# Performance work log

Hardware: AMD Instinct MI355X
Metric: run time of the kernel (lower is better)

## Reference

```python
import jax, jax.numpy as jnp
import numpy as np

N_ATOM_FEATS = 64
N_RBF = 10
N_CONV = 3
N_HIDDEN = 64
N_NODES = 50000
N_EDGES = 800000
N_GRAPHS = 512


def setup_inputs() -> dict:
    key = jax.random.key(0)
    ks = jax.random.split(key, 32)
    d = {}
    d["x_ids"] = jax.random.randint(ks[0], (N_NODES,), 0, 95)
    d["edge_index"] = jax.random.randint(ks[1], (2, N_EDGES), 0, N_NODES)
    d["edge_attr"] = jax.random.uniform(ks[2], (N_EDGES,), jnp.float32) * 6.0  # distances in [0,6)
    d["batch"] = jnp.sort(jax.random.randint(ks[3], (N_NODES,), 0, N_GRAPHS))
    # parameters
    def lin(k, fan_in, shape):
        return jax.random.normal(k, shape, jnp.float32) / np.sqrt(fan_in)
    d["emb"] = jax.random.normal(ks[4], (95, N_ATOM_FEATS), jnp.float32)
    d["blk_W1"] = lin(ks[5], N_ATOM_FEATS, (N_CONV, N_ATOM_FEATS, N_ATOM_FEATS))
    d["blk_b1"] = jnp.zeros((N_CONV, N_ATOM_FEATS), jnp.float32)
    d["blk_We"] = lin(ks[6], N_RBF, (N_CONV, N_RBF, N_ATOM_FEATS))
    d["blk_be"] = jnp.zeros((N_CONV, N_ATOM_FEATS), jnp.float32)
    d["blk_W2"] = lin(ks[7], N_ATOM_FEATS, (N_CONV, N_ATOM_FEATS, N_ATOM_FEATS))
    d["blk_b2"] = jnp.zeros((N_CONV, N_ATOM_FEATS), jnp.float32)
    d["Ws"] = lin(ks[8], N_ATOM_FEATS, (N_ATOM_FEATS, 2 * N_HIDDEN))
    d["bs"] = jnp.zeros((2 * N_HIDDEN,), jnp.float32)
    d["Wbg1"] = lin(ks[9], 2 * N_HIDDEN, (2 * N_HIDDEN, N_HIDDEN))
    d["bbg1"] = jnp.zeros((N_HIDDEN,), jnp.float32)
    d["Wbg2"] = lin(ks[10], N_HIDDEN, (N_HIDDEN, 1))
    d["bbg2"] = jnp.zeros((1,), jnp.float32)
    d["Weh1"] = lin(ks[11], 2 * N_HIDDEN, (2 * N_HIDDEN, N_HIDDEN))
    d["beh1"] = jnp.zeros((N_HIDDEN,), jnp.float32)
    d["Weh2"] = lin(ks[12], N_HIDDEN, (N_HIDDEN, 1))
    d["beh2"] = jnp.zeros((1,), jnp.float32)
    return d


def reference(x_ids, edge_index, edge_attr, batch, emb,
              blk_W1, blk_b1, blk_We, blk_be, blk_W2, blk_b2,
              Ws, bs, Wbg1, bbg1, Wbg2, bbg2, Weh1, beh1, Weh2, beh2):
    src, dst = edge_index[0], edge_index[1]
    # embedding lookup [N, F]
    x = emb[x_ids]
    # Gaussian smearing RBF: [E, n_rbf]
    offset = jnp.linspace(0.0, 6.0, N_RBF).astype(edge_attr.dtype)
    coeff = -0.5 / (offset[1] - offset[0]) ** 2
    e = jnp.exp(coeff * (edge_attr[:, None] - offset) ** 2)
    # interaction blocks (SchNet-style CFConv with residual)
    for i in range(N_CONV):
        h = x @ blk_W1[i] + blk_b1[i]                     # [N, F]
        f = e @ blk_We[i] + blk_be[i]                     # [E, F] edge filters
        m = h[src] * f                                    # [E, F] messages
        agg = jax.ops.segment_sum(m, dst, num_segments=N_NODES)
        x = x + agg @ blk_W2[i] + blk_b2[i]
        x = jax.nn.softplus(x)
    # global mean pool over graphs
    sums = jax.ops.segment_sum(x, batch, num_segments=N_GRAPHS)
    cnts = jax.ops.segment_sum(jnp.ones((x.shape[0],), x.dtype), batch, num_segments=N_GRAPHS)
    c = sums / jnp.maximum(cnts, 1.0)[:, None]
    c = jax.nn.relu(c @ Ws + bs)                          # [G, 2H]
    out_bg = jax.nn.relu(c @ Wbg1 + bbg1) @ Wbg2 + bbg2   # [G, 1]
    out_eh = jax.nn.relu(c @ Weh1 + beh1) @ Weh2 + beh2   # [G, 1]
    return (out_bg, out_eh)
```

## Files before the change

### kernel.cpp

```cpp
#include <hip/hip_runtime.h>
#include <hip/hip_fp16.h>
#include <cstddef>


#define RBF_C0 1.0f
#define RBF_C1 0.60653065971f
#define RBF_C2 0.13533528324f
#define RBF_C3 0.011108996538f
#define RBF_C4 3.3546262790e-4f
#define RBF_C5 3.7266531720e-6f
#define RBF_C6 1.5229979745e-8f
#define RBF_C7 2.2897348457e-11f
#define RBF_C8 1.2664165549e-14f
#define RBF_C9 2.5767043600e-18f

__device__ __forceinline__ float softplusf(float v) {
    return fmaxf(v, 0.0f) + log1pf(__expf(-fabsf(v)));
}

__device__ __forceinline__ float row_gemv(const float4* __restrict__ xr,
                                          const float w[64], float bj) {
    float a0 = bj, a1 = 0.f, a2 = 0.f, a3 = 0.f;
#pragma unroll
    for (int q = 0; q < 4; ++q) {
        float4 v0 = xr[4 * q + 0], v1 = xr[4 * q + 1];
        float4 v2 = xr[4 * q + 2], v3 = xr[4 * q + 3];
        a0 = fmaf(v0.x, w[16 * q + 0], a0);  a0 = fmaf(v0.y, w[16 * q + 1], a0);
        a0 = fmaf(v0.z, w[16 * q + 2], a0);  a0 = fmaf(v0.w, w[16 * q + 3], a0);
        a1 = fmaf(v1.x, w[16 * q + 4], a1);  a1 = fmaf(v1.y, w[16 * q + 5], a1);
        a1 = fmaf(v1.z, w[16 * q + 6], a1);  a1 = fmaf(v1.w, w[16 * q + 7], a1);
        a2 = fmaf(v2.x, w[16 * q + 8], a2);  a2 = fmaf(v2.y, w[16 * q + 9], a2);
        a2 = fmaf(v2.z, w[16 * q + 10], a2); a2 = fmaf(v2.w, w[16 * q + 11], a2);
        a3 = fmaf(v3.x, w[16 * q + 12], a3); a3 = fmaf(v3.y, w[16 * q + 13], a3);
        a3 = fmaf(v3.z, w[16 * q + 14], a3); a3 = fmaf(v3.w, w[16 * q + 15], a3);
    }
    return (a0 + a1) + (a2 + a3);
}

__device__ __forceinline__ float filt_ab(const float wp[10], float bj, float A, float B) {
    float P = wp[9];
    P = fmaf(B, P, wp[8]); P = fmaf(B, P, wp[7]); P = fmaf(B, P, wp[6]);
    P = fmaf(B, P, wp[5]); P = fmaf(B, P, wp[4]); P = fmaf(B, P, wp[3]);
    P = fmaf(B, P, wp[2]); P = fmaf(B, P, wp[1]); P = fmaf(B, P, wp[0]);
    return fmaf(A, P, bj);
}

__global__ void k_pre(const int* __restrict__ dst, int* __restrict__ deg,
                      const int* __restrict__ batch, int* __restrict__ gstart,
                      const int* __restrict__ ids, const float* __restrict__ emb,
                      const float* __restrict__ W1, const float* __restrict__ b1,
                      float* __restrict__ x, __half* __restrict__ hA,
                      int n_edges, int n_nodes, int n_graphs) {
    int tid = blockIdx.x * blockDim.x + threadIdx.x;
    int nth = gridDim.x * blockDim.x;
    for (int e = tid; e < n_edges; e += nth) atomicAdd(&deg[dst[e]], 1);
    for (int n = tid; n < n_nodes; n += nth) {
        int b = batch[n];
        int prev = (n == 0) ? -1 : batch[n - 1];
        for (int g = prev + 1; g <= b; ++g) gstart[g] = n;
        if (n == n_nodes - 1)
            for (int g = b + 1; g <= n_graphs; ++g) gstart[g] = n_nodes;
    }
    int lane = threadIdx.x & 63;
    int gw = __builtin_amdgcn_readfirstlane(tid >> 6);
    int nw = nth >> 6;
    float w[64];
#pragma unroll
    for (int k = 0; k < 64; ++k) w[k] = W1[k * 64 + lane];
    float bj = b1[lane];
    for (int n = gw; n < n_nodes; n += nw) {
        int id = __builtin_amdgcn_readfirstlane(ids[n]);
        const float4* xr = (const float4*)(emb + id * 64);
        float v = row_gemv(xr, w, bj);
        x[n * 64 + lane] = emb[id * 64 + lane];
        hA[n * 64 + lane] = __float2half(v);
    }
}

__global__ void k_scana(const int* __restrict__ deg, int* __restrict__ off_,
                        int* __restrict__ bsum, int n) {
    __shared__ int s[256];
    int i = blockIdx.x * 256 + threadIdx.x;
    int v = (i < n) ? deg[i] : 0;
    s[threadIdx.x] = v;
    __syncthreads();
    for (int off = 1; off < 256; off <<= 1) {
        int t = (threadIdx.x >= off) ? s[threadIdx.x - off] : 0;
        __syncthreads();
        s[threadIdx.x] += t;
        __syncthreads();
    }
    if (i < n) off_[i + 1] = s[threadIdx.x];
    if (threadIdx.x == 255) bsum[blockIdx.x] = s[255];
}

__global__ void k_scanb(int* __restrict__ bsum, int nb) {
    __shared__ int s[256];
    int v = ((int)threadIdx.x < nb) ? bsum[threadIdx.x] : 0;
    s[threadIdx.x] = v;
    __syncthreads();
    for (int off = 1; off < 256; off <<= 1) {
        int t = (threadIdx.x >= off) ? s[threadIdx.x - off] : 0;
        __syncthreads();
        s[threadIdx.x] += t;
        __syncthreads();
    }
    if ((int)threadIdx.x < nb) bsum[threadIdx.x] = s[threadIdx.x] - v;
}

__global__ void k_scanc(const int* __restrict__ deg, const int* __restrict__ bsum,
                        int* __restrict__ off_, int* __restrict__ cursor, int n) {
    int i = blockIdx.x * blockDim.x + threadIdx.x;
    if (i < n) {
        int incl = off_[i + 1] + bsum[i >> 8];
        off_[i + 1] = incl;
        cursor[i] = incl - deg[i];
    }
    if (i == 0) off_[0] = 0;
}

__global__ void k_scatter(const int* __restrict__ src, const int* __restrict__ dst,
                          const float* __restrict__ dist, int* __restrict__ cursor,
                          int4* __restrict__ psort, int n_edges) {
    int e = blockIdx.x * blockDim.x + threadIdx.x;
    if (e >= n_edges) return;
    int t = dst[e];
    int pos = atomicAdd(&cursor[t], 1);
    float d = dist[e];
    float A = __expf(-1.125f * d * d);
    float B = __expf(1.5f * d);
    psort[pos] = make_int4(src[e] << 6, __float_as_int(A), __float_as_int(B), 0);
}

__global__ __launch_bounds__(256, 4) void k_gemm(
        const float* __restrict__ X, const float* __restrict__ W,
        const float* __restrict__ bias, __half* __restrict__ Y, int n_nodes) {
    int lane = threadIdx.x & 63;
    int gw = __builtin_amdgcn_readfirstlane((blockIdx.x * blockDim.x + threadIdx.x) >> 6);
    int nw = (gridDim.x * blockDim.x) >> 6;
    float w[64];
#pragma unroll
    for (int k = 0; k < 64; ++k) w[k] = W[k * 64 + lane];
    float bj = bias[lane];
    for (int n = gw; n < n_nodes; n += nw) {
        const float4* xr = (const float4*)(X + n * 64);
        Y[n * 64 + lane] = __float2half(row_gemv(xr, w, bj));
    }
}

__global__ __launch_bounds__(256, 6) void k_conv(
        const int4* __restrict__ ps, const int* __restrict__ off,
        const __half* __restrict__ h,
        const float* __restrict__ We, const float* __restrict__ be,
        const float* __restrict__ W2, const float* __restrict__ b2,
        float* __restrict__ x, int n_nodes) {
    int lane = threadIdx.x & 63;
    int gw = __builtin_amdgcn_readfirstlane((blockIdx.x * blockDim.x + threadIdx.x) >> 6);
    int nw = (gridDim.x * blockDim.x) >> 6;

    const float C[10] = {RBF_C0, RBF_C1, RBF_C2, RBF_C3, RBF_C4,
                         RBF_C5, RBF_C6, RBF_C7, RBF_C8, RBF_C9};
    float wp[10];
#pragma unroll
    for (int r = 0; r < 10; ++r) wp[r] = We[r * 64 + lane] * C[r];
    float bj  = be[lane];
    float b2j = b2[lane];

    for (int n = gw; n < n_nodes; n += nw) {
        int k0 = __builtin_amdgcn_readfirstlane(off[n]);
        int k1 = __builtin_amdgcn_readfirstlane(off[n + 1]);
        float acc = 0.0f;
        int k = k0;
        for (; k + 8 <= k1; k += 8) {
            int4 p0 = ps[k + 0], p1 = ps[k + 1], p2 = ps[k + 2], p3 = ps[k + 3];
            int4 p4 = ps[k + 4], p5 = ps[k + 5], p6 = ps[k + 6], p7 = ps[k + 7];
            float g0 = __half2float(h[p0.x + lane]);
            float g1 = __half2float(h[p1.x + lane]);
            float g2 = __half2float(h[p2.x + lane]);
            float g3 = __half2float(h[p3.x + lane]);
            float g4 = __half2float(h[p4.x + lane]);
            float g5 = __half2float(h[p5.x + lane]);
            float g6 = __half2float(h[p6.x + lane]);
            float g7 = __half2float(h[p7.x + lane]);
            acc = fmaf(g0, filt_ab(wp, bj, __int_as_float(p0.y), __int_as_float(p0.z)), acc);
            acc = fmaf(g1, filt_ab(wp, bj, __int_as_float(p1.y), __int_as_float(p1.z)), acc);
            acc = fmaf(g2, filt_ab(wp, bj, __int_as_float(p2.y), __int_as_float(p2.z)), acc);
            acc = fmaf(g3, filt_ab(wp, bj, __int_as_float(p3.y), __int_as_float(p3.z)), acc);
            acc = fmaf(g4, filt_ab(wp, bj, __int_as_float(p4.y), __int_as_float(p4.z)), acc);
            acc = fmaf(g5, filt_ab(wp, bj, __int_as_float(p5.y), __int_as_float(p5.z)), acc);
            acc = fmaf(g6, filt_ab(wp, bj, __int_as_float(p6.y), __int_as_float(p6.z)), acc);
            acc = fmaf(g7, filt_ab(wp, bj, __int_as_float(p7.y), __int_as_float(p7.z)), acc);
        }
        for (; k + 4 <= k1; k += 4) {
            int4 p0 = ps[k + 0], p1 = ps[k + 1], p2 = ps[k + 2], p3 = ps[k + 3];
            float g0 = __half2float(h[p0.x + lane]);
            float g1 = __half2float(h[p1.x + lane]);
            float g2 = __half2float(h[p2.x + lane]);
            float g3 = __half2float(h[p3.x + lane]);
            acc = fmaf(g0, filt_ab(wp, bj, __int_as_float(p0.y), __int_as_float(p0.z)), acc);
            acc = fmaf(g1, filt_ab(wp, bj, __int_as_float(p1.y), __int_as_float(p1.z)), acc);
            acc = fmaf(g2, filt_ab(wp, bj, __int_as_float(p2.y), __int_as_float(p2.z)), acc);
            acc = fmaf(g3, filt_ab(wp, bj, __int_as_float(p3.y), __int_as_float(p3.z)), acc);
        }
        for (; k < k1; ++k) {
            int4 p = ps[k];
            float g = __half2float(h[p.x + lane]);
            acc = fmaf(g, filt_ab(wp, bj, __int_as_float(p.y), __int_as_float(p.z)), acc);
        }
        float o0 = b2j + x[n * 64 + lane];
        float o1 = 0.f, o2 = 0.f, o3 = 0.f;
#pragma unroll 4
        for (int kk = 0; kk < 16; ++kk) {
            o0 = fmaf(__shfl(acc, kk),      W2[(kk)      * 64 + lane], o0);
            o1 = fmaf(__shfl(acc, kk + 16), W2[(kk + 16) * 64 + lane], o1);
            o2 = fmaf(__shfl(acc, kk + 32), W2[(kk + 32) * 64 + lane], o2);
            o3 = fmaf(__shfl(acc, kk + 48), W2[(kk + 48) * 64 + lane], o3);
        }
        x[n * 64 + lane] = softplusf((o0 + o1) + (o2 + o3));
    }
}

__global__ void k_poolhead(const float* __restrict__ x, const int* __restrict__ gstart,
                           const float* __restrict__ Ws, const float* __restrict__ bs,
                           const float* __restrict__ Wbg1, const float* __restrict__ bbg1,
                           const float* __restrict__ Wbg2, const float* __restrict__ bbg2,
                           const float* __restrict__ Weh1, const float* __restrict__ beh1,
                           const float* __restrict__ Weh2, const float* __restrict__ beh2,
                           float* __restrict__ out, int n_graphs) {
    __shared__ float red[256];
    __shared__ float c[64];
    __shared__ float h1[128];
    int g = blockIdx.x;
    int t = threadIdx.x, j = t & 63, part = t >> 6;
    int s0 = gstart[g], s1 = gstart[g + 1];
    float acc = 0.0f;
    for (int n = s0 + part; n < s1; n += 4) acc += x[n * 64 + j];
    red[t] = acc;
    __syncthreads();
    if (part == 0)
        c[j] = (red[j] + red[64 + j] + red[128 + j] + red[192 + j]) /
               fmaxf((float)(s1 - s0), 1.0f);
    __syncthreads();
    if (t < 128) {
        float av = bs[t];
#pragma unroll 8
        for (int k = 0; k < 64; ++k) av = fmaf(c[k], Ws[k * 128 + t], av);
        h1[t] = fmaxf(av, 0.0f);
    }
    __syncthreads();
    if (t < 128) {
        const float* W1p = (t < 64) ? Wbg1 : Weh1;
        const float* b1p = (t < 64) ? bbg1 : beh1;
        const float* W2p = (t < 64) ? Wbg2 : Weh2;
        float b2v = (t < 64) ? bbg2[0] : beh2[0];
        int ln = t & 63;
        float a2 = b1p[ln];
#pragma unroll 8
        for (int k = 0; k < 128; ++k) a2 = fmaf(h1[k], W1p[k * 64 + ln], a2);
        a2 = fmaxf(a2, 0.0f);
        float pr = a2 * W2p[ln];
#pragma unroll
        for (int off = 32; off > 0; off >>= 1) pr += __shfl_down(pr, off);
        if (ln == 0) out[(t < 64 ? 0 : n_graphs) + g] = pr + b2v;
    }
}

extern "C" void kernel_launch(void* const* d_in, const int* in_sizes, int n_in,
                              void* d_out, int out_size, void* d_ws, size_t ws_size,
                              hipStream_t stream) {
    const int*   x_ids = (const int*)d_in[0];
    const int*   eidx  = (const int*)d_in[1];
    const float* eattr = (const float*)d_in[2];
    const int*   batch = (const int*)d_in[3];
    const float* emb   = (const float*)d_in[4];
    const float* W1    = (const float*)d_in[5];
    const float* b1    = (const float*)d_in[6];
    const float* We    = (const float*)d_in[7];
    const float* be    = (const float*)d_in[8];
    const float* W2    = (const float*)d_in[9];
    const float* b2    = (const float*)d_in[10];
    const float* Ws_   = (const float*)d_in[11];
    const float* bs_   = (const float*)d_in[12];
    const float* Wbg1  = (const float*)d_in[13];
    const float* bbg1  = (const float*)d_in[14];
    const float* Wbg2  = (const float*)d_in[15];
    const float* bbg2  = (const float*)d_in[16];
    const float* Weh1  = (const float*)d_in[17];
    const float* beh1  = (const float*)d_in[18];
    const float* Weh2  = (const float*)d_in[19];
    const float* beh2  = (const float*)d_in[20];

    int n_nodes  = in_sizes[0];
    int n_edges  = in_sizes[2];
    int n_graphs = out_size / 2;
    const int* src = eidx;
    const int* dst = eidx + n_edges;

    char* p = (char*)d_ws;
    float* x     = (float*)p;   p += (size_t)n_nodes * 64 * sizeof(float);
    __half* hA   = (__half*)p;  p += (size_t)n_nodes * 64 * sizeof(__half);
    __half* hB   = (__half*)p;  p += (size_t)n_nodes * 64 * sizeof(__half);
    int4* psort  = (int4*)p;    p += (size_t)n_edges * sizeof(int4);
    int* deg     = (int*)p;     p += (size_t)n_nodes * sizeof(int);
    int* off_    = (int*)p;     p += (size_t)(n_nodes + 1) * sizeof(int);
    int* cursor  = (int*)p;     p += (size_t)n_nodes * sizeof(int);
    int* bsum    = (int*)p;     p += 256 * sizeof(int);
    int* gstart  = (int*)p;     p += (size_t)(n_graphs + 1) * sizeof(int);
    float* out   = (float*)d_out;

    int nchunks = (n_nodes + 255) / 256;
    int nbE = (n_edges + 255) / 256;
    int nbN = (n_nodes + 255) / 256;

    hipMemsetAsync(deg, 0, (size_t)n_nodes * sizeof(int), stream);
    k_pre<<<nbE, 256, 0, stream>>>(dst, deg, batch, gstart, x_ids, emb, W1, b1,
                                   x, hA, n_edges, n_nodes, n_graphs);
    k_scana<<<nchunks, 256, 0, stream>>>(deg, off_, bsum, n_nodes);
    k_scanb<<<1, 256, 0, stream>>>(bsum, nchunks);
    k_scanc<<<nbN, 256, 0, stream>>>(deg, bsum, off_, cursor, n_nodes);
    k_scatter<<<nbE, 256, 0, stream>>>(src, dst, eattr, cursor, psort, n_edges);

    k_conv<<<4096, 256, 0, stream>>>(psort, off_, hA, We, be, W2, b2, x, n_nodes);
    k_gemm<<<1024, 256, 0, stream>>>(x, W1 + 4096, b1 + 64, hB, n_nodes);
    k_conv<<<4096, 256, 0, stream>>>(psort, off_, hB, We + 640, be + 64,
                                     W2 + 4096, b2 + 64, x, n_nodes);
    k_gemm<<<1024, 256, 0, stream>>>(x, W1 + 8192, b1 + 128, hA, n_nodes);
    k_conv<<<4096, 256, 0, stream>>>(psort, off_, hA, We + 1280, be + 128,
                                     W2 + 8192, b2 + 128, x, n_nodes);

    k_poolhead<<<n_graphs, 256, 0, stream>>>(x, gstart, Ws_, bs_, Wbg1, bbg1, Wbg2, bbg2,
                                             Weh1, beh1, Weh2, beh2, out, n_graphs);
}
```

Measured before the change: 462.4 us.

## Split edge records into SoA and process two edges per wave with half2 gathers

The packed int4 edge record is replaced by separate src-index and (A,B) float2 arrays, which removes the unused padding word from edge traffic. In k_conv each wave is split into two 32-lane halves that handle alternate edges, each lane computing two features and reading them with a __half2 load. The two halves are combined with a shuffle before the W2 projection. This halves the loop trip count and widens the gathers, at the cost of doubled filter registers and an extra cross-half reduction.

Result: slower. 543.0 us (+17.4%).

```diff
diff --git a/kernel.cpp b/kernel.cpp
--- a/kernel.cpp
+++ b/kernel.cpp
@@ -35,14 +35,6 @@
         a3 = fmaf(v3.z, w[16 * q + 14], a3); a3 = fmaf(v3.w, w[16 * q + 15], a3);
     }
     return (a0 + a1) + (a2 + a3);
-}
-
-__device__ __forceinline__ float filt_ab(const float wp[10], float bj, float A, float B) {
-    float P = wp[9];
-    P = fmaf(B, P, wp[8]); P = fmaf(B, P, wp[7]); P = fmaf(B, P, wp[6]);
-    P = fmaf(B, P, wp[5]); P = fmaf(B, P, wp[4]); P = fmaf(B, P, wp[3]);
-    P = fmaf(B, P, wp[2]); P = fmaf(B, P, wp[1]); P = fmaf(B, P, wp[0]);
-    return fmaf(A, P, bj);
 }
 
 __global__ void k_pre(const int* __restrict__ dst, int* __restrict__ deg,
@@ -121,7 +113,7 @@
 
 __global__ void k_scatter(const int* __restrict__ src, const int* __restrict__ dst,
                           const float* __restrict__ dist, int* __restrict__ cursor,
-                          int4* __restrict__ psort, int n_edges) {
+                          int* __restrict__ srcs, float2* __restrict__ ab, int n_edges) {
     int e = blockIdx.x * blockDim.x + threadIdx.x;
     if (e >= n_edges) return;
     int t = dst[e];
@@ -129,7 +121,8 @@
     float d = dist[e];
     float A = __expf(-1.125f * d * d);
     float B = __expf(1.5f * d);
-    psort[pos] = make_int4(src[e] << 6, __float_as_int(A), __float_as_int(B), 0);
+    srcs[pos] = src[e] << 6;
+    ab[pos] = make_float2(A, B);
 }
 
 __global__ __launch_bounds__(256, 4) void k_gemm(
@@ -148,73 +141,96 @@
     }
 }
 
+__device__ __forceinline__ void edge_acc(const float wpx[10], const float wpy[10],
+                                         float bex, float bey,
+                                         float A, float B, float2 g,
+                                         float& ax, float& ay) {
+    float Px = wpx[9], Py = wpy[9];
+    Px = fmaf(B, Px, wpx[8]); Py = fmaf(B, Py, wpy[8]);
+    Px = fmaf(B, Px, wpx[7]); Py = fmaf(B, Py, wpy[7]);
+    Px = fmaf(B, Px, wpx[6]); Py = fmaf(B, Py, wpy[6]);
+    Px = fmaf(B, Px, wpx[5]); Py = fmaf(B, Py, wpy[5]);
+    Px = fmaf(B, Px, wpx[4]); Py = fmaf(B, Py, wpy[4]);
+    Px = fmaf(B, Px, wpx[3]); Py = fmaf(B, Py, wpy[3]);
+    Px = fmaf(B, Px, wpx[2]); Py = fmaf(B, Py, wpy[2]);
+    Px = fmaf(B, Px, wpx[1]); Py = fmaf(B, Py, wpy[1]);
+    Px = fmaf(B, Px, wpx[0]); Py = fmaf(B, Py, wpy[0]);
+    float fx = fmaf(A, Px, bex);
+    float fy = fmaf(A, Py, bey);
+    ax = fmaf(g.x, fx, ax);
+    ay = fmaf(g.y, fy, ay);
+}
+
 __global__ __launch_bounds__(256, 6) void k_conv(
-        const int4* __restrict__ ps, const int* __restrict__ off,
-        const __half* __restrict__ h,
+        const int* __restrict__ srcs, const float2* __restrict__ ab,
+        const int* __restrict__ off, const __half* __restrict__ h,
         const float* __restrict__ We, const float* __restrict__ be,
         const float* __restrict__ W2, const float* __restrict__ b2,
         float* __restrict__ x, int n_nodes) {
     int lane = threadIdx.x & 63;
+    int half = lane >> 5;
+    int fl   = lane & 31;
+    int f0   = fl << 1;
     int gw = __builtin_amdgcn_readfirstlane((blockIdx.x * blockDim.x + threadIdx.x) >> 6);
     int nw = (gridDim.x * blockDim.x) >> 6;
 
     const float C[10] = {RBF_C0, RBF_C1, RBF_C2, RBF_C3, RBF_C4,
                          RBF_C5, RBF_C6, RBF_C7, RBF_C8, RBF_C9};
-    float wp[10];
-#pragma unroll
-    for (int r = 0; r < 10; ++r) wp[r] = We[r * 64 + lane] * C[r];
-    float bj  = be[lane];
+    float wpx[10], wpy[10];
+#pragma unroll
+    for (int r = 0; r < 10; ++r) {
+        wpx[r] = We[r * 64 + f0] * C[r];
+        wpy[r] = We[r * 64 + f0 + 1] * C[r];
+    }
+    float bex = be[f0], bey = be[f0 + 1];
     float b2j = b2[lane];
 
     for (int n = gw; n < n_nodes; n += nw) {
         int k0 = __builtin_amdgcn_readfirstlane(off[n]);
         int k1 = __builtin_amdgcn_readfirstlane(off[n + 1]);
-        float acc = 0.0f;
+        float ax = 0.f, ay = 0.f;
         int k = k0;
         for (; k + 8 <= k1; k += 8) {
-            int4 p0 = ps[k + 0], p1 = ps[k + 1], p2 = ps[k + 2], p3 = ps[k + 3];
-            int4 p4 = ps[k + 4], p5 = ps[k + 5], p6 = ps[k + 6], p7 = ps[k + 7];
-            float g0 = __half2float(h[p0.x + lane]);
-            float g1 = __half2float(h[p1.x + lane]);
-            float g2 = __half2float(h[p2.x + lane]);
-            float g3 = __half2float(h[p3.x + lane]);
-            float g4 = __half2float(h[p4.x + lane]);
-            float g5 = __half2float(h[p5.x + lane]);
-            float g6 = __half2float(h[p6.x + lane]);
-            float g7 = __half2float(h[p7.x + lane]);
-            acc = fmaf(g0, filt_ab(wp, bj, __int_as_float(p0.y), __int_as_float(p0.z)), acc);
-            acc = fmaf(g1, filt_ab(wp, bj, __int_as_float(p1.y), __int_as_float(p1.z)), acc);
-            acc = fmaf(g2, filt_ab(wp, bj, __int_as_float(p2.y), __int_as_float(p2.z)), acc);
-            acc = fmaf(g3, filt_ab(wp, bj, __int_as_float(p3.y), __int_as_float(p3.z)), acc);
-            acc = fmaf(g4, filt_ab(wp, bj, __int_as_float(p4.y), __int_as_float(p4.z)), acc);
-            acc = fmaf(g5, filt_ab(wp, bj, __int_as_float(p5.y), __int_as_float(p5.z)), acc);
-            acc = fmaf(g6, filt_ab(wp, bj, __int_as_float(p6.y), __int_as_float(p6.z)), acc);
-            acc = fmaf(g7, filt_ab(wp, bj, __int_as_float(p7.y), __int_as_float(p7.z)), acc);
+            int e0 = k + half, e1 = k + 2 + half, e2 = k + 4 + half, e3 = k + 6 + half;
+            int s0 = srcs[e0], s1 = srcs[e1], s2 = srcs[e2], s3 = srcs[e3];
+            float2 ab0 = ab[e0], ab1 = ab[e1], ab2 = ab[e2], ab3 = ab[e3];
+            float2 g0 = __half22float2(*(const __half2*)(h + s0 + f0));
+            float2 g1 = __half22float2(*(const __half2*)(h + s1 + f0));
+            float2 g2 = __half22float2(*(const __half2*)(h + s2 + f0));
+            float2 g3 = __half22float2(*(const __half2*)(h + s3 + f0));
+            edge_acc(wpx, wpy, bex, bey, ab0.x, ab0.y, g0, ax, ay);
+            edge_acc(wpx, wpy, bex, bey, ab1.x, ab1.y, g1, ax, ay);
+            edge_acc(wpx, wpy, bex, bey, ab2.x, ab2.y, g2, ax, ay);
+            edge_acc(wpx, wpy, bex, bey, ab3.x, ab3.y, g3, ax, ay);
         }
-        for (; k + 4 <= k1; k += 4) {
-            int4 p0 = ps[k + 0], p1 = ps[k + 1], p2 = ps[k + 2], p3 = ps[k + 3];
-            float g0 = __half2float(h[p0.x + lane]);
-            float g1 = __half2float(h[p1.x + lane]);
-            float g2 = __half2float(h[p2.x + lane]);
-            float g3 = __half2float(h[p3.x + lane]);
-            acc = fmaf(g0, filt_ab(wp, bj, __int_as_float(p0.y), __int_as_float(p0.z)), acc);
-            acc = fmaf(g1, filt_ab(wp, bj, __int_as_float(p1.y), __int_as_float(p1.z)), acc);
-            acc = fmaf(g2, filt_ab(wp, bj, __int_as_float(p2.y), __int_as_float(p2.z)), acc);
-            acc = fmaf(g3, filt_ab(wp, bj, __int_as_float(p3.y), __int_as_float(p3.z)), acc);
+        for (; k + 2 <= k1; k += 2) {
+            int e = k + half;
+            int s = srcs[e];
+            float2 abv = ab[e];
+            float2 g = __half22float2(*(const __half2*)(h + s + f0));
+            edge_acc(wpx, wpy, bex, bey, abv.x, abv.y, g, ax, ay);
         }
-        for (; k < k1; ++k) {
-            int4 p = ps[k];
-            float g = __half2float(h[p.x + lane]);
-            acc = fmaf(g, filt_ab(wp, bj, __int_as_float(p.y), __int_as_float(p.z)), acc);
+        if (k < k1 && half == 0) {
+            int e = k1 - 1;
+            int s = srcs[e];
+            float2 abv = ab[e];
+            float2 g = __half22float2(*(const __half2*)(h + s + f0));
+            edge_acc(wpx, wpy, bex, bey, abv.x, abv.y, g, ax, ay);
         }
+        ax += __shfl(ax, fl + 32);
+        ay += __shfl(ay, fl + 32);
         float o0 = b2j + x[n * 64 + lane];
         float o1 = 0.f, o2 = 0.f, o3 = 0.f;
 #pragma unroll 4
         for (int kk = 0; kk < 16; ++kk) {
-            o0 = fmaf(__shfl(acc, kk),      W2[(kk)      * 64 + lane], o0);
-            o1 = fmaf(__shfl(acc, kk + 16), W2[(kk + 16) * 64 + lane], o1);
-            o2 = fmaf(__shfl(acc, kk + 32), W2[(kk + 32) * 64 + lane], o2);
-            o3 = fmaf(__shfl(acc, kk + 48), W2[(kk + 48) * 64 + lane], o3);
+            float v0 = __shfl((kk & 1) ? ay : ax, kk >> 1);
+            float v1 = __shfl(((kk + 16) & 1) ? ay : ax, (kk + 16) >> 1);
+            float v2 = __shfl(((kk + 32) & 1) ? ay : ax, (kk + 32) >> 1);
+            float v3 = __shfl(((kk + 48) & 1) ? ay : ax, (kk + 48) >> 1);
+            o0 = fmaf(v0, W2[(kk)      * 64 + lane], o0);
+            o1 = fmaf(v1, W2[(kk + 16) * 64 + lane], o1);
+            o2 = fmaf(v2, W2[(kk + 32) * 64 + lane], o2);
+            o3 = fmaf(v3, W2[(kk + 48) * 64 + lane], o3);
         }
         x[n * 64 + lane] = softplusf((o0 + o1) + (o2 + o3));
     }
@@ -300,7 +316,8 @@
     float* x     = (float*)p;   p += (size_t)n_nodes * 64 * sizeof(float);
     __half* hA   = (__half*)p;  p += (size_t)n_nodes * 64 * sizeof(__half);
     __half* hB   = (__half*)p;  p += (size_t)n_nodes * 64 * sizeof(__half);
-    int4* psort  = (int4*)p;    p += (size_t)n_edges * sizeof(int4);
+    int* srcs    = (int*)p;     p += (size_t)n_edges * sizeof(int);
+    float2* ab   = (float2*)p;  p += (size_t)n_edges * sizeof(float2);
     int* deg     = (int*)p;     p += (size_t)n_nodes * sizeof(int);
     int* off_    = (int*)p;     p += (size_t)(n_nodes + 1) * sizeof(int);
     int* cursor  = (int*)p;     p += (size_t)n_nodes * sizeof(int);
@@ -318,14 +335,14 @@
     k_scana<<<nchunks, 256, 0, stream>>>(deg, off_, bsum, n_nodes);
     k_scanb<<<1, 256, 0, stream>>>(bsum, nchunks);
     k_scanc<<<nbN, 256, 0, stream>>>(deg, bsum, off_, cursor, n_nodes);
-    k_scatter<<<nbE, 256, 0, stream>>>(src, dst, eattr, cursor, psort, n_edges);
-
-    k_conv<<<4096, 256, 0, stream>>>(psort, off_, hA, We, be, W2, b2, x, n_nodes);
+    k_scatter<<<nbE, 256, 0, stream>>>(src, dst, eattr, cursor, srcs, ab, n_edges);
+
+    k_conv<<<4096, 256, 0, stream>>>(srcs, ab, off_, hA, We, be, W2, b2, x, n_nodes);
     k_gemm<<<1024, 256, 0, stream>>>(x, W1 + 4096, b1 + 64, hB, n_nodes);
-    k_conv<<<4096, 256, 0, stream>>>(psort, off_, hB, We + 640, be + 64,
+    k_conv<<<4096, 256, 0, stream>>>(srcs, ab, off_, hB, We + 640, be + 64,
                                      W2 + 4096, b2 + 64, x, n_nodes);
     k_gemm<<<1024, 256, 0, stream>>>(x, W1 + 8192, b1 + 128, hA, n_nodes);
-    k_conv<<<4096, 256, 0, stream>>>(psort, off_, hA, We + 1280, be + 128,
+    k_conv<<<4096, 256, 0, stream>>>(srcs, ab, off_, hA, We + 1280, be + 128,
                                      W2 + 8192, b2 + 128, x, n_nodes);
 
     k_poolhead<<<n_graphs, 256, 0, stream>>>(x, gstart, Ws_, bs_, Wbg1, bbg1, Wbg2, bbg2,
```
